# Optimization experiments

Hardware: AMD Instinct MI355X
Metric: run time of the kernel (lower is better)

Reference implementation:

```python
import jax, jax.numpy as jnp
from jax import lax
import numpy as np

EPS_BN = 1e-5


def _bn(x, g, b, axis):
    # eval-mode BatchNorm with running_mean=0, running_var=1
    shape = [1] * x.ndim
    shape[axis] = -1
    scale = (g / jnp.sqrt(1.0 + EPS_BN)).reshape(shape)
    return x * scale + b.reshape(shape)


def farthest_point_sample(xyz, npoint):
    B, N, _ = xyz.shape
    bidx = jnp.arange(B)

    def body(carry, _):
        dist, far = carry                      # [B,N], [B]
        centroid = xyz[bidx, far]              # [B,3]
        d = jnp.sum((xyz - centroid[:, None, :]) ** 2, axis=-1)
        dist = jnp.minimum(dist, d)
        return (dist, jnp.argmax(dist, axis=-1)), far

    init = (jnp.full((B, N), 1e10, xyz.dtype), jnp.zeros((B,), jnp.int32))
    _, idxs = lax.scan(body, init, None, length=npoint)
    return idxs.T                              # [B,npoint]


def square_distance(src, dst):
    # [B,S,3] x [B,N,3] -> [B,S,N]
    d = -2.0 * jnp.einsum('bsc,bnc->bsn', src, dst)
    d = d + jnp.sum(src ** 2, -1)[:, :, None] + jnp.sum(dst ** 2, -1)[:, None, :]
    return d


def sample_and_group(npoint, nsample, xyz, points):
    B = xyz.shape[0]
    bidx = jnp.arange(B)
    fps_idx = farthest_point_sample(xyz, npoint)          # [B,S]
    new_xyz = xyz[bidx[:, None], fps_idx]                 # [B,S,3]
    new_points = points[bidx[:, None], fps_idx]           # [B,S,C]
    dists = square_distance(new_xyz, xyz)                 # [B,S,N]
    _, idx = lax.top_k(-dists, nsample)                   # nearest nsample
    grouped = points[bidx[:, None, None], idx]            # [B,S,K,C]
    grouped_norm = grouped - new_points[:, :, None, :]
    rep = jnp.broadcast_to(new_points[:, :, None, :], grouped.shape)
    return new_xyz, jnp.concatenate([grouped_norm, rep], axis=-1)  # [B,S,K,2C]


def local_op(x, w, g, b):
    # x [B,S,K,D]; conv1d k=1 over channels D, BN, ReLU, max over K -> [B,out,S]
    y = jnp.einsum('bskd,od->bsko', x, w)
    y = jax.nn.relu(_bn(y, g, b, axis=3))
    y = jnp.max(y, axis=2)                                # [B,S,out]
    return jnp.transpose(y, (0, 2, 1))                    # [B,out,S]


def sa_layer(x, qk_w, v_w, v_b, t_w, t_b, g, b):
    # x [B,C,N]; q and k share weights (offset attention)
    xq = jnp.einsum('bcn,oc->bno', x, qk_w)               # [B,N,C/4]
    xk = jnp.einsum('bcn,oc->bon', x, qk_w)               # [B,C/4,N]
    xv = jnp.einsum('bcn,oc->bon', x, v_w) + v_b[:, None]
    energy = jnp.einsum('bnd,bdm->bnm', xq, xk)           # [B,N,N]
    attn = jax.nn.softmax(energy, axis=-1)
    attn = attn / (1e-9 + attn.sum(axis=1, keepdims=True))
    x_r = jnp.einsum('bcn,bnm->bcm', xv, attn)
    x_r = jnp.einsum('bcn,oc->bon', x - x_r, t_w) + t_b[:, None]
    x_r = jax.nn.relu(_bn(x_r, g, b, axis=1))
    return x + x_r


def setup_inputs() -> dict:
    key = jax.random.key(0)
    ks = iter(jax.random.split(key, 48))
    rn = lambda shape, s=0.05: jax.random.normal(next(ks), shape, jnp.float32) * s
    inp = {
        'xyz': jax.random.normal(next(ks), (32, 16384, 3), jnp.float32),
        'f': jax.random.normal(next(ks), (32, 16384, 3), jnp.float32),
        'conv1_w': rn((64, 6)), 'bn1_g': jnp.ones(64), 'bn1_b': jnp.zeros(64),
        'l0_w': rn((64, 128)), 'l0_g': jnp.ones(64), 'l0_b': jnp.zeros(64),
        'l1_w': rn((64, 128)), 'l1_g': jnp.ones(64), 'l1_b': jnp.zeros(64),
        'st_c1_w': rn((64, 64)), 'st_bn1_g': jnp.ones(64), 'st_bn1_b': jnp.zeros(64),
        'st_c2_w': rn((64, 64)), 'st_bn2_g': jnp.ones(64), 'st_bn2_b': jnp.zeros(64),
        'sa1_qk_w': rn((16, 64)), 'sa1_v_w': rn((64, 64)), 'sa1_v_b': jnp.zeros(64),
        'sa1_t_w': rn((64, 64)), 'sa1_t_b': jnp.zeros(64), 'sa1_g': jnp.ones(64), 'sa1_b': jnp.zeros(64),
        'sa2_qk_w': rn((16, 64)), 'sa2_v_w': rn((64, 64)), 'sa2_v_b': jnp.zeros(64),
        'sa2_t_w': rn((64, 64)), 'sa2_t_b': jnp.zeros(64), 'sa2_g': jnp.ones(64), 'sa2_b': jnp.zeros(64),
        'fuse_w': rn((256, 192)), 'fuse_g': jnp.ones(256), 'fuse_b': jnp.zeros(256),
        'lin1_w': rn((256, 256)), 'bn6_g': jnp.ones(256), 'bn6_b': jnp.zeros(256),
        'lin2_w': rn((256, 256)), 'lin2_b': jnp.zeros(256),
    }
    return inp


def _forward(xyz, f, conv1_w, bn1_g, bn1_b, l0_w, l0_g, l0_b, l1_w, l1_g, l1_b,
             st_c1_w, st_bn1_g, st_bn1_b, st_c2_w, st_bn2_g, st_bn2_b,
             sa1_qk_w, sa1_v_w, sa1_v_b, sa1_t_w, sa1_t_b, sa1_g, sa1_b,
             sa2_qk_w, sa2_v_w, sa2_v_b, sa2_t_w, sa2_t_b, sa2_g, sa2_b,
             fuse_w, fuse_g, fuse_b, lin1_w, bn6_g, bn6_b, lin2_w, lin2_b):
    center = jnp.mean(xyz, axis=1)                        # [B,3]
    xyz_c = xyz - center[:, None, :]
    pts = jnp.concatenate([xyz_c, f], axis=2)             # [B,N,6]
    geo = pts[..., :3]
    xin = jnp.transpose(pts, (0, 2, 1))                   # [B,6,N]
    x = jax.nn.relu(_bn(jnp.einsum('bcn,oc->bon', xin, conv1_w), bn1_g, bn1_b, 1))
    x = jnp.transpose(x, (0, 2, 1))                       # [B,N,64]
    new_xyz, nf = sample_and_group(128, 32, geo, x)
    feature_0 = local_op(nf, l0_w, l0_g, l0_b)            # [B,64,128]
    feature = jnp.transpose(feature_0, (0, 2, 1))
    _, nf2 = sample_and_group(32, 16, new_xyz, feature)
    feature_1 = local_op(nf2, l1_w, l1_g, l1_b)           # [B,64,32]
    # StackedAttention
    x = jax.nn.relu(_bn(jnp.einsum('bcn,oc->bon', feature_1, st_c1_w), st_bn1_g, st_bn1_b, 1))
    x = jax.nn.relu(_bn(jnp.einsum('bcn,oc->bon', x, st_c2_w), st_bn2_g, st_bn2_b, 1))
    x1 = sa_layer(x, sa1_qk_w, sa1_v_w, sa1_v_b, sa1_t_w, sa1_t_b, sa1_g, sa1_b)
    x2 = sa_layer(x1, sa2_qk_w, sa2_v_w, sa2_v_b, sa2_t_w, sa2_t_b, sa2_g, sa2_b)
    x = jnp.concatenate([x1, x2], axis=1)                 # [B,128,32]
    x = jnp.concatenate([x, feature_1], axis=1)           # [B,192,32]
    x = jax.nn.leaky_relu(_bn(jnp.einsum('bcn,oc->bon', x, fuse_w), fuse_g, fuse_b, 1), 0.2)
    x = jnp.max(x, axis=2)                                # [B,256]
    x = jax.nn.relu(_bn(x @ lin1_w.T, bn6_g, bn6_b, 1))   # dropout = identity (eval)
    x = x @ lin2_w.T + lin2_b
    return center, x


def reference(xyz, f, conv1_w, bn1_g, bn1_b, l0_w, l0_g, l0_b, l1_w, l1_g, l1_b,
              st_c1_w, st_bn1_g, st_bn1_b, st_c2_w, st_bn2_g, st_bn2_b,
              sa1_qk_w, sa1_v_w, sa1_v_b, sa1_t_w, sa1_t_b, sa1_g, sa1_b,
              sa2_qk_w, sa2_v_w, sa2_v_b, sa2_t_w, sa2_t_b, sa2_g, sa2_b,
              fuse_w, fuse_g, fuse_b, lin1_w, bn6_g, bn6_b, lin2_w, lin2_b):
    return _forward(xyz, f, conv1_w, bn1_g, bn1_b, l0_w, l0_g, l0_b, l1_w, l1_g, l1_b,
                    st_c1_w, st_bn1_g, st_bn1_b, st_c2_w, st_bn2_g, st_bn2_b,
                    sa1_qk_w, sa1_v_w, sa1_v_b, sa1_t_w, sa1_t_b, sa1_g, sa1_b,
                    sa2_qk_w, sa2_v_w, sa2_v_b, sa2_t_w, sa2_t_b, sa2_g, sa2_b,
                    fuse_w, fuse_g, fuse_b, lin1_w, bn6_g, bn6_b, lin2_w, lin2_b)
```

## Files before the change

kernel.cpp:

```cpp
#include <hip/hip_runtime.h>


__device__ __forceinline__ float bnscale(float g){ return g / sqrtf(1.0f + 1e-5f); }

__device__ __forceinline__ float conv_feat6(float p0,float p1,float p2,float p3,float p4,float p5,
                                            float w0,float w1,float w2,float w3,float w4,float w5,
                                            float sc,float bs){
    float y = p0*w0;
    y = fmaf(p1,w1,y); y = fmaf(p2,w2,y); y = fmaf(p3,w3,y);
    y = fmaf(p4,w4,y); y = fmaf(p5,w5,y);
    return fmaxf(fmaf(y,sc,bs), 0.0f);
}

__device__ __forceinline__ float fpsdist(float dx,float dy,float dz){
    #pragma clang fp contract(off)
    return (dx*dx + dy*dy) + dz*dz;
}

__device__ __forceinline__ float sumsq3(float x,float y,float z){
    #pragma clang fp contract(off)
    return (x*x + y*y) + z*z;
}
__device__ __forceinline__ float sqdist3(float qx,float qy,float qz,float qs,
                                         float px,float py,float pz){
    #pragma clang fp contract(off)
    {
        float dot = (qx*px + qy*py) + qz*pz;
        float pn  = (px*px + py*py) + pz*pz;
        return (-2.0f*dot + qs) + pn;
    }
}

__device__ __forceinline__ unsigned long long packdi(float d, unsigned int idx){
    unsigned int u = __float_as_uint(d);
    unsigned int msk = (unsigned int)((int)u >> 31);
    u ^= (msk | 0x80000000u);
    return ((unsigned long long)u << 32) | (unsigned long long)idx;
}

__device__ __forceinline__ unsigned long long u64min(unsigned long long a, unsigned long long b){
    return a < b ? a : b;
}

__device__ __forceinline__ unsigned long long u64_shfl_down(unsigned long long v, int off){
    unsigned int lo = (unsigned int)v, hi = (unsigned int)(v >> 32);
    lo = __shfl_down(lo, off, 64);
    hi = __shfl_down(hi, off, 64);
    return ((unsigned long long)hi << 32) | (unsigned long long)lo;
}

__device__ __forceinline__ unsigned long long u64_bcast0(unsigned long long v){
    unsigned int lo = (unsigned int)v, hi = (unsigned int)(v >> 32);
    lo = __shfl(lo, 0, 64);
    hi = __shfl(hi, 0, 64);
    return ((unsigned long long)hi << 32) | (unsigned long long)lo;
}

__global__ __launch_bounds__(512, 1) void k_fps1(const float* __restrict__ xyz,
                                                 float* __restrict__ center,
                                                 float* __restrict__ out,
                                                 int* __restrict__ idx_out){
    constexpr int NTH = 512, PPT = 32, N = 16384, NPOINT = 128, NW = 8;
    int b = blockIdx.x, t = threadIdx.x;
    int wid = t>>6, lane = t&63;

    __shared__ float s_red[NW][3];
    __shared__ unsigned int s_khi[2][NW], s_klo[2][NW];

    const float* xb = xyz + (size_t)b*N*3;
    float px[PPT], py[PPT], pz[PPT], dist[PPT];
    #pragma unroll
    for (int i=0;i<PPT;i++){
        const float* sp = xb + (size_t)(t + i*NTH)*3;
        px[i]=sp[0]; py[i]=sp[1]; pz[i]=sp[2];
        dist[i]=1e10f;
    }
    float sx=0.f, sy=0.f, sz=0.f;
    #pragma unroll
    for (int i=0;i<PPT;i++){ sx+=px[i]; sy+=py[i]; sz+=pz[i]; }
    #pragma unroll
    for (int off=32; off>=1; off>>=1){
        sx += __shfl_down(sx, off, 64);
        sy += __shfl_down(sy, off, 64);
        sz += __shfl_down(sz, off, 64);
    }
    if (lane==0){ s_red[wid][0]=sx; s_red[wid][1]=sy; s_red[wid][2]=sz; }
    __syncthreads();
    float cx0=0.f, cy0=0.f, cz0=0.f;
    #pragma unroll
    for (int w2=0; w2<NW; ++w2){ cx0+=s_red[w2][0]; cy0+=s_red[w2][1]; cz0+=s_red[w2][2]; }
    cx0 *= (1.0f/16384.0f); cy0 *= (1.0f/16384.0f); cz0 *= (1.0f/16384.0f);
    if (t < 3){
        float c = (t==0)?cx0:((t==1)?cy0:cz0);
        center[b*3+t] = c;
        out[b*3+t] = c;
    }
    #pragma unroll
    for (int i=0;i<PPT;i++){ px[i]-=cx0; py[i]-=cy0; pz[i]-=cz0; }
    if (t==0) idx_out[b*NPOINT] = 0;

    float cx = xb[0]-cx0, cy = xb[1]-cy0, cz = xb[2]-cz0;

    for (int it=1; it<NPOINT; ++it){
        int par = it & 1;
        float bv = -1.0f; int bis = 0;
        #pragma unroll
        for (int i=0;i<PPT;i++){
            float d = fpsdist(px[i]-cx, py[i]-cy, pz[i]-cz);
            float nd = fminf(dist[i], d);
            dist[i] = nd;
            bool better = nd > bv;
            bv  = better ? nd : bv;
            bis = better ? i  : bis;
        }
        int bi = t + (bis<<9);
        unsigned long long key = ((unsigned long long)__float_as_uint(bv) << 32)
                               | (unsigned long long)(unsigned)(~(unsigned)bi);
        #pragma unroll
        for (int off=32; off>=1; off>>=1){
            unsigned long long ok = u64_shfl_down(key, off);
            key = ok > key ? ok : key;
        }
        if (lane==0){ s_khi[par][wid]=(unsigned)(key>>32); s_klo[par][wid]=(unsigned)key; }
        __syncthreads();
        unsigned long long gk = ((unsigned long long)s_khi[par][0] << 32) | s_klo[par][0];
        #pragma unroll
        for (int w2=1; w2<NW; ++w2){
            unsigned long long k2 = ((unsigned long long)s_khi[par][w2] << 32) | s_klo[par][w2];
            if (k2 > gk) gk = k2;
        }
        int gi = (int)(~(unsigned)(gk & 0xFFFFFFFFull));
        gi = __builtin_amdgcn_readfirstlane(gi);
        if (t==0) idx_out[b*NPOINT + it] = gi;
        const float* wp = xb + (size_t)gi*3;
        cx = wp[0]-cx0; cy = wp[1]-cy0; cz = wp[2]-cz0;
    }
}

__global__ __launch_bounds__(256) void k_knn1(const float* __restrict__ xyz,
                                              const float* __restrict__ f,
                                              const float* __restrict__ center,
                                              const float* __restrict__ conv1_w,
                                              const float* __restrict__ bn1_g,
                                              const float* __restrict__ bn1_b,
                                              const int* __restrict__ fps_idx,
                                              float* __restrict__ new_xyz,
                                              float* __restrict__ np_feat,
                                              int* __restrict__ knn_idx){
    int t = threadIdx.x, wid = t>>6, lane = t&63;
    int q = blockIdx.x*4 + wid;
    int b = q>>7, s = q&127;

    float cx = center[b*3+0], cy = center[b*3+1], cz = center[b*3+2];
    int idx = fps_idx[b*128+s];
    const float* xp = xyz + ((size_t)b*16384 + idx)*3;
    const float* fp = f   + ((size_t)b*16384 + idx)*3;
    float p0 = xp[0]-cx, p1 = xp[1]-cy, p2 = xp[2]-cz;
    float p3 = fp[0], p4 = fp[1], p5 = fp[2];

    {
        const float* w6 = conv1_w + lane*6;
        float v = conv_feat6(p0,p1,p2,p3,p4,p5, w6[0],w6[1],w6[2],w6[3],w6[4],w6[5],
                             bnscale(bn1_g[lane]), bn1_b[lane]);
        np_feat[(size_t)q*64 + lane] = v;
        if (lane < 3){
            float pc = (lane==0)?p0:((lane==1)?p1:p2);
            new_xyz[(size_t)q*3 + lane] = pc;
        }
    }

    float qx = p0, qy = p1, qz = p2;
    float qs = sumsq3(qx,qy,qz);
    const float* xb = xyz + (size_t)b*16384*3;

    unsigned long long m0=~0ull, m1=~0ull, m2=~0ull, m3=~0ull;
    for (int i=0; i<256; i+=4){
        #pragma unroll
        for (int j=0;j<4;j++){
            int n = lane + ((i+j)<<6);
            const float* p = xb + (size_t)n*3;
            float dx = p[0]-cx, dy = p[1]-cy, dz = p[2]-cz;
            float d = sqdist3(qx,qy,qz,qs,dx,dy,dz);
            unsigned long long pk = packdi(d,(unsigned)n);
            if (j==0) m0 = u64min(m0,pk);
            else if (j==1) m1 = u64min(m1,pk);
            else if (j==2) m2 = u64min(m2,pk);
            else m3 = u64min(m3,pk);
        }
    }

    size_t kbase = (size_t)q*32;
    for (int r=0; r<32; ++r){
        unsigned long long mm = u64min(u64min(m0,m1), u64min(m2,m3));
        #pragma unroll
        for (int off=32; off>=1; off>>=1) mm = u64min(mm, u64_shfl_down(mm, off));
        unsigned long long win = u64_bcast0(mm);
        unsigned int widx = (unsigned int)(win & 0xFFFFFFFFull);
        if (lane==0) knn_idx[kbase + r] = (int)widx;
        int c = (int)(widx & 255u);
        int n2 = c + (lane<<8);
        const float* p = xb + (size_t)n2*3;
        float dx = p[0]-cx, dy = p[1]-cy, dz = p[2]-cz;
        float d = sqdist3(qx,qy,qz,qs,dx,dy,dz);
        unsigned long long pk = packdi(d,(unsigned)n2);
        if (pk <= win) pk = ~0ull;
        #pragma unroll
        for (int off=32; off>=1; off>>=1) pk = u64min(pk, u64_shfl_down(pk, off));
        unsigned long long nm = u64_bcast0(pk);
        int owner = c & 63, slot = c >> 6;
        if (lane == owner){
            if (slot==0) m0 = nm;
            else if (slot==1) m1 = nm;
            else if (slot==2) m2 = nm;
            else m3 = nm;
        }
    }
}

template<int K, int NQ, int NSRC, bool RECOMP>
__global__ __launch_bounds__(256, 2) void k_group_local(
    const float* __restrict__ xyz, const float* __restrict__ f, const float* __restrict__ center,
    const float* __restrict__ conv1_w, const float* __restrict__ bn1_g, const float* __restrict__ bn1_b,
    const float* __restrict__ src_feat,
    const int* __restrict__ knn_idx, const float* __restrict__ np_feat,
    const float* __restrict__ w, const float* __restrict__ g, const float* __restrict__ bb,
    float* __restrict__ out)
{
    __shared__ float wt[128*65];
    __shared__ float s_sc[64], s_bs[64];
    __shared__ float cwT[6*64];
    __shared__ float s_csc[64], s_cbs[64];
    __shared__ float np_l[4][64];
    __shared__ float gda[4][K][64];
    __shared__ float s_pts[4][K][6];

    int t = threadIdx.x;
    for (int e=t; e<8192; e+=256){ int o = e>>7, d = e&127; wt[d*65 + o] = w[e]; }
    if (t < 64){ s_sc[t] = bnscale(g[t]); s_bs[t] = bb[t]; }
    if constexpr (RECOMP){
        for (int e=t; e<384; e+=256){ int o = e/6, j = e%6; cwT[j*64 + o] = conv1_w[e]; }
        if (t < 64){ s_csc[t] = bnscale(bn1_g[t]); s_cbs[t] = bn1_b[t]; }
    }
    __syncthreads();

    int wid = t>>6, lane = t&63;
    int q = blockIdx.x*4 + wid;
    int b = q / NQ, s = q % NQ;

    float np_o = np_feat[((size_t)b*NQ + s)*64 + lane];
    np_l[wid][lane] = np_o;

    const int* kix = knn_idx + ((size_t)b*NQ + s)*K;

    if constexpr (RECOMP){
        float cx = center[b*3+0], cy = center[b*3+1], cz = center[b*3+2];
        if (lane < K){
            int myi = kix[lane];
            const float* xp = xyz + ((size_t)b*16384 + myi)*3;
            s_pts[wid][lane][0] = xp[0]-cx;
            s_pts[wid][lane][1] = xp[1]-cy;
            s_pts[wid][lane][2] = xp[2]-cz;
            const float* fp = f + ((size_t)b*16384 + myi)*3;
            s_pts[wid][lane][3] = fp[0];
            s_pts[wid][lane][4] = fp[1];
            s_pts[wid][lane][5] = fp[2];
        }
        #pragma unroll
        for (int k=0; k<K; ++k){
            float gv = conv_feat6(s_pts[wid][k][0], s_pts[wid][k][1], s_pts[wid][k][2],
                                  s_pts[wid][k][3], s_pts[wid][k][4], s_pts[wid][k][5],
                                  cwT[0*64+lane], cwT[1*64+lane], cwT[2*64+lane],
                                  cwT[3*64+lane], cwT[4*64+lane], cwT[5*64+lane],
                                  s_csc[lane], s_cbs[lane]);
            gda[wid][k][lane] = gv - np_o;
        }
    } else {
        int myi = kix[lane < K ? lane : 0];
        #pragma unroll
        for (int k=0; k<K; ++k){
            int ik = __shfl(myi, k, 64);
            gda[wid][k][lane] = src_feat[((size_t)b*NSRC + ik)*64 + lane] - np_o;
        }
    }

    float C = 0.f;
    #pragma unroll
    for (int d=0; d<64; d++) C = fmaf(np_l[wid][d], wt[(64+d)*65 + lane], C);

    float acc_y[K];
    #pragma unroll
    for (int k=0;k<K;k++) acc_y[k] = C;

    #pragma unroll
    for (int c=0; c<2; ++c){
        float wr[32];
        #pragma unroll
        for (int j=0;j<32;j++) wr[j] = wt[(c*32+j)*65 + lane];
        #pragma unroll
        for (int k=0;k<K;k++){
            const float4* g4 = (const float4*)&gda[wid][k][c*32];
            float yk = 0.f;
            #pragma unroll
            for (int j4=0;j4<8;j4++){
                float4 gg = g4[j4];
                yk = fmaf(gg.x, wr[j4*4+0], yk);
                yk = fmaf(gg.y, wr[j4*4+1], yk);
                yk = fmaf(gg.z, wr[j4*4+2], yk);
                yk = fmaf(gg.w, wr[j4*4+3], yk);
            }
            acc_y[k] = acc_y[k] + yk;
        }
    }

    float acc = -1e30f;
    #pragma unroll
    for (int k=0;k<K;k++){
        float v = fmaxf(fmaf(acc_y[k], s_sc[lane], s_bs[lane]), 0.0f);
        acc = fmaxf(acc, v);
    }
    out[((size_t)b*NQ + s)*64 + lane] = acc;
}

__device__ void sa_block(const float* X, float* Xout,
                         float* Q, float* E, float* XV, float* XR, float* CS,
                         const float* qk_w, const float* v_w, const float* v_b,
                         const float* t_w, const float* t_b,
                         const float* g, const float* bb, int t)
{
    for (int e=t; e<512; e+=256){
        int n = e>>4, o = e&15;
        float y = 0.f;
        for (int c=0;c<64;c++) y = fmaf(qk_w[o*64+c], X[c*32+n], y);
        Q[n*16+o] = y;
    }
    for (int e=t; e<2048; e+=256){
        int o = e>>5, n = e&31;
        float y = v_b[o];
        for (int c=0;c<64;c++) y = fmaf(v_w[o*64+c], X[c*32+n], y);
        XV[o*32+n] = y;
    }
    __syncthreads();
    for (int e=t; e<1024; e+=256){
        int n = e>>5, m = e&31;
        float y = 0.f;
        for (int d=0;d<16;d++) y = fmaf(Q[n*16+d], Q[m*16+d], y);
        E[e] = y;
    }
    __syncthreads();
    if (t < 32){
        float mx = -1e30f;
        for (int m=0;m<32;m++) mx = fmaxf(mx, E[t*32+m]);
        float sum = 0.f;
        for (int m=0;m<32;m++){ float v = expf(E[t*32+m]-mx); E[t*32+m]=v; sum += v; }
        for (int m=0;m<32;m++) E[t*32+m] = E[t*32+m] / sum;
    }
    __syncthreads();
    if (t < 32){
        float cs = 0.f;
        for (int n=0;n<32;n++) cs += E[n*32+t];
        CS[t] = 1e-9f + cs;
    }
    __syncthreads();
    for (int e=t; e<1024; e+=256) E[e] = E[e] / CS[e&31];
    __syncthreads();
    for (int e=t; e<2048; e+=256){
        int c = e>>5, m = e&31;
        float y = 0.f;
        for (int n=0;n<32;n++) y = fmaf(XV[c*32+n], E[n*32+m], y);
        XR[c*32+m] = y;
    }
    __syncthreads();
    for (int e=t; e<2048; e+=256){
        int o = e>>5, n = e&31;
        float y = 0.f;
        for (int c=0;c<64;c++) y = fmaf(t_w[o*64+c], X[c*32+n]-XR[c*32+n], y);
        y += t_b[o];
        y = fmaxf(fmaf(y, bnscale(g[o]), bb[o]), 0.0f);
        Xout[e] = X[e] + y;
    }
    __syncthreads();
}

__global__ __launch_bounds__(256) void k_mega(
    const float* __restrict__ new_xyz1,
    const float* __restrict__ feat,
    const float* __restrict__ l1_w, const float* __restrict__ l1_g, const float* __restrict__ l1_b,
    const float* st_c1_w, const float* st_bn1_g, const float* st_bn1_b,
    const float* st_c2_w, const float* st_bn2_g, const float* st_bn2_b,
    const float* sa1_qk, const float* sa1_v, const float* sa1_vb,
    const float* sa1_t, const float* sa1_tb, const float* sa1_g, const float* sa1_b,
    const float* sa2_qk, const float* sa2_v, const float* sa2_vb,
    const float* sa2_t, const float* sa2_tb, const float* sa2_g, const float* sa2_b,
    const float* fuse_w, const float* fuse_g, const float* fuse_b,
    const float* lin1_w, const float* bn6_g, const float* bn6_b,
    const float* lin2_w, const float* lin2_b,
    float* __restrict__ out)
{
    __shared__ float nx1[384];
    __shared__ int   s_i2[32];
    __shared__ float np2L[2048];
    __shared__ float nx2[96];
    __shared__ int   s_k2[512];
    __shared__ float wt[8320];
    __shared__ float s_sc[64], s_bs[64];
    __shared__ float gdaL[4][16][64];
    __shared__ float smt[14848];

    int b = blockIdx.x, t = threadIdx.x, wid = t>>6, lane = t&63;

    for (int e=t; e<384; e+=256) nx1[e] = new_xyz1[(size_t)b*384 + e];
    for (int e=t; e<8192; e+=256){ int o = e>>7, d = e&127; wt[d*65 + o] = l1_w[e]; }
    if (t < 64){ s_sc[t] = bnscale(l1_g[t]); s_bs[t] = l1_b[t]; }
    __syncthreads();

    if (wid == 0){
        float px[2],py[2],pz[2],dist[2];
        #pragma unroll
        for (int i=0;i<2;i++){
            int n = lane + i*64;
            px[i]=nx1[n*3+0]; py[i]=nx1[n*3+1]; pz[i]=nx1[n*3+2];
            dist[i]=1e10f;
        }
        if (lane==0) s_i2[0] = 0;
        float cx=nx1[0], cy=nx1[1], cz=nx1[2];
        for (int it=1; it<32; ++it){
            float bv=-1.0f; int bi=0;
            float bx=0.f, by=0.f, bz=0.f;
            #pragma unroll
            for (int i=0;i<2;i++){
                float d = fpsdist(px[i]-cx, py[i]-cy, pz[i]-cz);
                float nd = fminf(dist[i], d);
                dist[i]=nd;
                bool better = nd > bv;
                bv = better ? nd : bv;
                bi = better ? (lane + i*64) : bi;
                bx = better ? px[i] : bx;
                by = better ? py[i] : by;
                bz = better ? pz[i] : bz;
            }
            unsigned long long key = ((unsigned long long)__float_as_uint(bv) << 32)
                                   | (unsigned long long)(unsigned)(~(unsigned)bi);
            #pragma unroll
            for (int off=32; off>=1; off>>=1){
                unsigned long long ok = u64_shfl_down(key, off);
                float ox = __shfl_down(bx, off, 64);
                float oy = __shfl_down(by, off, 64);
                float oz = __shfl_down(bz, off, 64);
                bool better = ok > key;
                key = better ? ok : key;
                bx = better ? ox : bx;
                by = better ? oy : by;
                bz = better ? oz : bz;
            }
            key = u64_bcast0(key);
            cx = __shfl(bx, 0, 64); cy = __shfl(by, 0, 64); cz = __shfl(bz, 0, 64);
            if (lane==0) s_i2[it] = (int)(~(unsigned)(key & 0xFFFFFFFFull));
        }
    }
    __syncthreads();

    for (int e=t; e<2048; e+=256){
        int s = e>>6, o = e&63;
        np2L[s*64 + o] = feat[((size_t)b*128 + s_i2[s])*64 + o];
    }
    if (t < 32){
        int idx = s_i2[t];
        nx2[t*3+0] = nx1[idx*3+0];
        nx2[t*3+1] = nx1[idx*3+1];
        nx2[t*3+2] = nx1[idx*3+2];
    }
    __syncthreads();

    for (int j=0;j<8;j++){
        int s = wid + 4*j;
        float qx = nx2[s*3+0], qy = nx2[s*3+1], qz = nx2[s*3+2];
        float qs = sumsq3(qx,qy,qz);
        unsigned long long pp0, pp1;
        {
            float ax=nx1[lane*3+0], ay=nx1[lane*3+1], az=nx1[lane*3+2];
            pp0 = packdi(sqdist3(qx,qy,qz,qs,ax,ay,az), (unsigned)lane);
            ax=nx1[(lane+64)*3+0]; ay=nx1[(lane+64)*3+1]; az=nx1[(lane+64)*3+2];
            pp1 = packdi(sqdist3(qx,qy,qz,qs,ax,ay,az), (unsigned)(lane+64));
        }
        for (int r=0; r<16; ++r){
            unsigned long long mm = u64min(pp0, pp1);
            #pragma unroll
            for (int off=32; off>=1; off>>=1) mm = u64min(mm, u64_shfl_down(mm, off));
            unsigned long long win = u64_bcast0(mm);
            if (lane==0) s_k2[s*16 + r] = (int)(win & 0xFFFFFFFFull);
            if (pp0 == win) pp0 = ~0ull;
            if (pp1 == win) pp1 = ~0ull;
        }
    }
    __syncthreads();

    for (int j=0;j<8;j++){
        int s = wid + 4*j;
        float np_o = np2L[s*64 + lane];
        #pragma unroll
        for (int k=0;k<16;k++){
            int ik = s_k2[s*16 + k];
            gdaL[wid][k][lane] = feat[((size_t)b*128 + ik)*64 + lane] - np_o;
        }
        float C0 = 0.f;
        #pragma unroll
        for (int d=0; d<64; d++) C0 = fmaf(np2L[s*64 + d], wt[(64+d)*65 + lane], C0);
        float acc_y[16];
        #pragma unroll
        for (int k=0;k<16;k++) acc_y[k] = C0;
        #pragma unroll
        for (int c=0; c<2; ++c){
            float wr[32];
            #pragma unroll
            for (int jj=0;jj<32;jj++) wr[jj] = wt[(c*32+jj)*65 + lane];
            #pragma unroll
            for (int k=0;k<16;k++){
                const float4* g4 = (const float4*)&gdaL[wid][k][c*32];
                float yk = 0.f;
                #pragma unroll
                for (int j4=0;j4<8;j4++){
                    float4 gg = g4[j4];
                    yk = fmaf(gg.x, wr[j4*4+0], yk);
                    yk = fmaf(gg.y, wr[j4*4+1], yk);
                    yk = fmaf(gg.z, wr[j4*4+2], yk);
                    yk = fmaf(gg.w, wr[j4*4+3], yk);
                }
                acc_y[k] = acc_y[k] + yk;
            }
        }
        float acc = -1e30f;
        #pragma unroll
        for (int k=0;k<16;k++){
            float v = fmaxf(fmaf(acc_y[k], s_sc[lane], s_bs[lane]), 0.0f);
            acc = fmaxf(acc, v);
        }
        smt[lane*32 + s] = acc;
    }
    __syncthreads();

    float* F1 = smt;
    float* XA = smt + 2048;
    float* XB = smt + 4096;
    float* Q  = smt + 6144;
    float* E  = smt + 6656;
    float* XV = smt + 7680;
    float* XR = smt + 9728;
    float* CS = smt + 11776;
    float* FO = smt + 6144;
    float* PO = smt + 14336;
    float* P2 = smt + 14592;

    for (int e=t; e<2048; e+=256){
        int o = e>>5, n = e&31;
        float y = 0.f;
        for (int c=0;c<64;c++) y = fmaf(st_c1_w[o*64+c], F1[c*32+n], y);
        XA[e] = fmaxf(fmaf(y, bnscale(st_bn1_g[o]), st_bn1_b[o]), 0.0f);
    }
    __syncthreads();
    for (int e=t; e<2048; e+=256){
        int o = e>>5, n = e&31;
        float y = 0.f;
        for (int c=0;c<64;c++) y = fmaf(st_c2_w[o*64+c], XA[c*32+n], y);
        XB[e] = fmaxf(fmaf(y, bnscale(st_bn2_g[o]), st_bn2_b[o]), 0.0f);
    }
    __syncthreads();
    sa_block(XB, XA, Q,E,XV,XR,CS, sa1_qk, sa1_v, sa1_vb, sa1_t, sa1_tb, sa1_g, sa1_b, t);
    sa_block(XA, XB, Q,E,XV,XR,CS, sa2_qk, sa2_v, sa2_vb, sa2_t, sa2_tb, sa2_g, sa2_b, t);
    for (int e=t; e<8192; e+=256){
        int o = e>>5, n = e&31;
        const float* wr = fuse_w + o*192;
        float y = 0.f;
        for (int c=0;c<64;c++) y = fmaf(wr[c],      XA[c*32+n], y);
        for (int c=0;c<64;c++) y = fmaf(wr[64+c],   XB[c*32+n], y);
        for (int c=0;c<64;c++) y = fmaf(wr[128+c],  F1[c*32+n], y);
        float v = fmaf(y, bnscale(fuse_g[o]), fuse_b[o]);
        FO[e] = (v > 0.0f) ? v : 0.2f*v;
    }
    __syncthreads();
    {
        float mx = -1e30f;
        for (int n=0;n<32;n++) mx = fmaxf(mx, FO[t*32+n]);
        PO[t] = mx;
    }
    __syncthreads();
    {
        const float* wr = lin1_w + t*256;
        float y = 0.f;
        for (int c=0;c<256;c++) y = fmaf(wr[c], PO[c], y);
        P2[t] = fmaxf(fmaf(y, bnscale(bn6_g[t]), bn6_b[t]), 0.0f);
    }
    __syncthreads();
    {
        const float* wr = lin2_w + t*256;
        float y = 0.f;
        for (int c=0;c<256;c++) y = fmaf(wr[c], P2[c], y);
        out[96 + b*256 + t] = y + lin2_b[t];
    }
}

extern "C" void kernel_launch(void* const* d_in, const int* in_sizes, int n_in,
                              void* d_out, int out_size, void* d_ws, size_t ws_size,
                              hipStream_t stream)
{
    const float* xyz      = (const float*)d_in[0];
    const float* f        = (const float*)d_in[1];
    const float* conv1_w  = (const float*)d_in[2];
    const float* bn1_g    = (const float*)d_in[3];
    const float* bn1_b    = (const float*)d_in[4];
    const float* l0_w     = (const float*)d_in[5];
    const float* l0_g     = (const float*)d_in[6];
    const float* l0_b     = (const float*)d_in[7];
    const float* l1_w     = (const float*)d_in[8];
    const float* l1_g     = (const float*)d_in[9];
    const float* l1_b     = (const float*)d_in[10];
    const float* st_c1_w  = (const float*)d_in[11];
    const float* st_bn1_g = (const float*)d_in[12];
    const float* st_bn1_b = (const float*)d_in[13];
    const float* st_c2_w  = (const float*)d_in[14];
    const float* st_bn2_g = (const float*)d_in[15];
    const float* st_bn2_b = (const float*)d_in[16];
    const float* sa1_qk   = (const float*)d_in[17];
    const float* sa1_v    = (const float*)d_in[18];
    const float* sa1_vb   = (const float*)d_in[19];
    const float* sa1_t    = (const float*)d_in[20];
    const float* sa1_tb   = (const float*)d_in[21];
    const float* sa1_g    = (const float*)d_in[22];
    const float* sa1_b    = (const float*)d_in[23];
    const float* sa2_qk   = (const float*)d_in[24];
    const float* sa2_v    = (const float*)d_in[25];
    const float* sa2_vb   = (const float*)d_in[26];
    const float* sa2_t    = (const float*)d_in[27];
    const float* sa2_tb   = (const float*)d_in[28];
    const float* sa2_g    = (const float*)d_in[29];
    const float* sa2_b    = (const float*)d_in[30];
    const float* fuse_w   = (const float*)d_in[31];
    const float* fuse_g   = (const float*)d_in[32];
    const float* fuse_b   = (const float*)d_in[33];
    const float* lin1_w   = (const float*)d_in[34];
    const float* bn6_g    = (const float*)d_in[35];
    const float* bn6_b    = (const float*)d_in[36];
    const float* lin2_w   = (const float*)d_in[37];
    const float* lin2_b   = (const float*)d_in[38];
    float* out = (float*)d_out;

    float* ws = (float*)d_ws;
    float* center   = ws + 0;
    float* new_xyz1 = ws + 96;
    float* np1      = ws + 12384;
    float* feat     = ws + 274528;
    int*   fps1     = (int*)(ws + 536672);
    int*   knn1     = (int*)(ws + 540768);

    k_fps1<<<32, 512, 0, stream>>>(xyz, center, out, fps1);
    k_knn1<<<1024, 256, 0, stream>>>(xyz, f, center, conv1_w, bn1_g, bn1_b,
                                     fps1, new_xyz1, np1, knn1);
    k_group_local<32,128,1,true><<<1024, 256, 0, stream>>>(
        xyz, f, center, conv1_w, bn1_g, bn1_b, nullptr, knn1, np1, l0_w, l0_g, l0_b, feat);
    k_mega<<<32, 256, 0, stream>>>(new_xyz1, feat,
        l1_w, l1_g, l1_b,
        st_c1_w, st_bn1_g, st_bn1_b, st_c2_w, st_bn2_g, st_bn2_b,
        sa1_qk, sa1_v, sa1_vb, sa1_t, sa1_tb, sa1_g, sa1_b,
        sa2_qk, sa2_v, sa2_vb, sa2_t, sa2_tb, sa2_g, sa2_b,
        fuse_w, fuse_g, fuse_b, lin1_w, bn6_g, bn6_b, lin2_w, lin2_b, out);
}
```

Measured before the change: 729.5 us.

## Widen FPS and mega kernels to 1024 threads with shuffle-based softmax

Doubles the FPS block to 1024 threads with 16 points per thread, and quadruples the mega kernel block to 1024 threads. The grid has only 32 blocks, so the aim is more parallelism per block to cut the latency of the serial FPS loop and the tail network. The attention softmax now uses wave shuffles instead of a 32-thread serial loop. Shared buffers are re-laid out with padded strides (33) to avoid bank conflicts, and the gathered-feature buffer is reused in halves. Risks are more waves taking part in each block-wide barrier and higher register pressure under the 1024-thread launch bounds.

```diff
diff --git a/kernel.cpp b/kernel.cpp
--- a/kernel.cpp
+++ b/kernel.cpp
@@ -56,11 +56,11 @@
     return ((unsigned long long)hi << 32) | (unsigned long long)lo;
 }
 
-__global__ __launch_bounds__(512, 1) void k_fps1(const float* __restrict__ xyz,
-                                                 float* __restrict__ center,
-                                                 float* __restrict__ out,
-                                                 int* __restrict__ idx_out){
-    constexpr int NTH = 512, PPT = 32, N = 16384, NPOINT = 128, NW = 8;
+__global__ __launch_bounds__(1024, 1) void k_fps1(const float* __restrict__ xyz,
+                                                  float* __restrict__ center,
+                                                  float* __restrict__ out,
+                                                  int* __restrict__ idx_out){
+    constexpr int NTH = 1024, PPT = 16, N = 16384, NPOINT = 128, NW = 16;
     int b = blockIdx.x, t = threadIdx.x;
     int wid = t>>6, lane = t&63;
 
@@ -113,7 +113,7 @@
             bv  = better ? nd : bv;
             bis = better ? i  : bis;
         }
-        int bi = t + (bis<<9);
+        int bi = t + (bis<<10);
         unsigned long long key = ((unsigned long long)__float_as_uint(bv) << 32)
                                | (unsigned long long)(unsigned)(~(unsigned)bi);
         #pragma unroll
@@ -327,32 +327,37 @@
                          const float* t_w, const float* t_b,
                          const float* g, const float* bb, int t)
 {
-    for (int e=t; e<512; e+=256){
+    constexpr int NT = 1024;
+    for (int e=t; e<512; e+=NT){
         int n = e>>4, o = e&15;
         float y = 0.f;
         for (int c=0;c<64;c++) y = fmaf(qk_w[o*64+c], X[c*32+n], y);
         Q[n*16+o] = y;
     }
-    for (int e=t; e<2048; e+=256){
+    for (int e=t; e<2048; e+=NT){
         int o = e>>5, n = e&31;
         float y = v_b[o];
         for (int c=0;c<64;c++) y = fmaf(v_w[o*64+c], X[c*32+n], y);
         XV[o*32+n] = y;
     }
     __syncthreads();
-    for (int e=t; e<1024; e+=256){
-        int n = e>>5, m = e&31;
+    {
+        int n = t>>5, m = t&31;
         float y = 0.f;
         for (int d=0;d<16;d++) y = fmaf(Q[n*16+d], Q[m*16+d], y);
-        E[e] = y;
-    }
-    __syncthreads();
-    if (t < 32){
-        float mx = -1e30f;
-        for (int m=0;m<32;m++) mx = fmaxf(mx, E[t*32+m]);
-        float sum = 0.f;
-        for (int m=0;m<32;m++){ float v = expf(E[t*32+m]-mx); E[t*32+m]=v; sum += v; }
-        for (int m=0;m<32;m++) E[t*32+m] = E[t*32+m] / sum;
+        E[t] = y;
+    }
+    __syncthreads();
+    {
+        float v = E[t];
+        float mx = v;
+        #pragma unroll
+        for (int mk=16; mk>=1; mk>>=1) mx = fmaxf(mx, __shfl_xor(mx, mk, 64));
+        float p = expf(v - mx);
+        float sum = p;
+        #pragma unroll
+        for (int mk=16; mk>=1; mk>>=1) sum += __shfl_xor(sum, mk, 64);
+        E[t] = p / sum;
     }
     __syncthreads();
     if (t < 32){
@@ -361,16 +366,16 @@
         CS[t] = 1e-9f + cs;
     }
     __syncthreads();
-    for (int e=t; e<1024; e+=256) E[e] = E[e] / CS[e&31];
-    __syncthreads();
-    for (int e=t; e<2048; e+=256){
+    E[t] = E[t] / CS[t&31];
+    __syncthreads();
+    for (int e=t; e<2048; e+=NT){
         int c = e>>5, m = e&31;
         float y = 0.f;
         for (int n=0;n<32;n++) y = fmaf(XV[c*32+n], E[n*32+m], y);
         XR[c*32+m] = y;
     }
     __syncthreads();
-    for (int e=t; e<2048; e+=256){
+    for (int e=t; e<2048; e+=NT){
         int o = e>>5, n = e&31;
         float y = 0.f;
         for (int c=0;c<64;c++) y = fmaf(t_w[o*64+c], X[c*32+n]-XR[c*32+n], y);
@@ -381,7 +386,7 @@
     __syncthreads();
 }
 
-__global__ __launch_bounds__(256) void k_mega(
+__global__ __launch_bounds__(1024) void k_mega(
     const float* __restrict__ new_xyz1,
     const float* __restrict__ feat,
     const float* __restrict__ l1_w, const float* __restrict__ l1_g, const float* __restrict__ l1_b,
@@ -396,6 +401,7 @@
     const float* lin2_w, const float* lin2_b,
     float* __restrict__ out)
 {
+    constexpr int NT = 1024;
     __shared__ float nx1[384];
     __shared__ int   s_i2[32];
     __shared__ float np2L[2048];
@@ -403,13 +409,12 @@
     __shared__ int   s_k2[512];
     __shared__ float wt[8320];
     __shared__ float s_sc[64], s_bs[64];
-    __shared__ float gdaL[4][16][64];
-    __shared__ float smt[14848];
+    __shared__ float smt[15168];
 
     int b = blockIdx.x, t = threadIdx.x, wid = t>>6, lane = t&63;
 
-    for (int e=t; e<384; e+=256) nx1[e] = new_xyz1[(size_t)b*384 + e];
-    for (int e=t; e<8192; e+=256){ int o = e>>7, d = e&127; wt[d*65 + o] = l1_w[e]; }
+    for (int e=t; e<384; e+=NT) nx1[e] = new_xyz1[(size_t)b*384 + e];
+    for (int e=t; e<8192; e+=NT){ int o = e>>7, d = e&127; wt[d*65 + o] = l1_w[e]; }
     if (t < 64){ s_sc[t] = bnscale(l1_g[t]); s_bs[t] = l1_b[t]; }
     __syncthreads();
 
@@ -459,7 +464,7 @@
     }
     __syncthreads();
 
-    for (int e=t; e<2048; e+=256){
+    for (int e=t; e<2048; e+=NT){
         int s = e>>6, o = e&63;
         np2L[s*64 + o] = feat[((size_t)b*128 + s_i2[s])*64 + o];
     }
@@ -471,8 +476,8 @@
     }
     __syncthreads();
 
-    for (int j=0;j<8;j++){
-        int s = wid + 4*j;
+    for (int j=0;j<2;j++){
+        int s = wid + 16*j;
         float qx = nx2[s*3+0], qy = nx2[s*3+1], qz = nx2[s*3+2];
         float qs = sumsq3(qx,qy,qz);
         unsigned long long pp0, pp1;
@@ -494,14 +499,10 @@
     }
     __syncthreads();
 
-    for (int j=0;j<8;j++){
-        int s = wid + 4*j;
+    float* gda = smt + 2112;
+    for (int j=0;j<2;j++){
+        int s = wid + 16*j;
         float np_o = np2L[s*64 + lane];
-        #pragma unroll
-        for (int k=0;k<16;k++){
-            int ik = s_k2[s*16 + k];
-            gdaL[wid][k][lane] = feat[((size_t)b*128 + ik)*64 + lane] - np_o;
-        }
         float C0 = 0.f;
         #pragma unroll
         for (int d=0; d<64; d++) C0 = fmaf(np2L[s*64 + d], wt[(64+d)*65 + lane], C0);
@@ -509,23 +510,31 @@
         #pragma unroll
         for (int k=0;k<16;k++) acc_y[k] = C0;
         #pragma unroll
-        for (int c=0; c<2; ++c){
-            float wr[32];
+        for (int half=0; half<2; ++half){
             #pragma unroll
-            for (int jj=0;jj<32;jj++) wr[jj] = wt[(c*32+jj)*65 + lane];
+            for (int kk=0;kk<8;++kk){
+                int ik = s_k2[s*16 + half*8 + kk];
+                gda[(wid*8+kk)*64 + lane] = feat[((size_t)b*128 + ik)*64 + lane] - np_o;
+            }
             #pragma unroll
-            for (int k=0;k<16;k++){
-                const float4* g4 = (const float4*)&gdaL[wid][k][c*32];
-                float yk = 0.f;
+            for (int c=0; c<2; ++c){
+                float wr[32];
                 #pragma unroll
-                for (int j4=0;j4<8;j4++){
-                    float4 gg = g4[j4];
-                    yk = fmaf(gg.x, wr[j4*4+0], yk);
-                    yk = fmaf(gg.y, wr[j4*4+1], yk);
-                    yk = fmaf(gg.z, wr[j4*4+2], yk);
-                    yk = fmaf(gg.w, wr[j4*4+3], yk);
+                for (int jj=0;jj<32;jj++) wr[jj] = wt[(c*32+jj)*65 + lane];
+                #pragma unroll
+                for (int kk=0;kk<8;++kk){
+                    const float4* g4 = (const float4*)&gda[(wid*8+kk)*64 + c*32];
+                    float yk = 0.f;
+                    #pragma unroll
+                    for (int j4=0;j4<8;j4++){
+                        float4 gg = g4[j4];
+                        yk = fmaf(gg.x, wr[j4*4+0], yk);
+                        yk = fmaf(gg.y, wr[j4*4+1], yk);
+                        yk = fmaf(gg.z, wr[j4*4+2], yk);
+                        yk = fmaf(gg.w, wr[j4*4+3], yk);
+                    }
+                    acc_y[half*8+kk] = acc_y[half*8+kk] + yk;
                 }
-                acc_y[k] = acc_y[k] + yk;
             }
         }
         float acc = -1e30f;
@@ -534,30 +543,30 @@
             float v = fmaxf(fmaf(acc_y[k], s_sc[lane], s_bs[lane]), 0.0f);
             acc = fmaxf(acc, v);
         }
-        smt[lane*32 + s] = acc;
+        smt[lane*33 + s] = acc;
     }
     __syncthreads();
 
     float* F1 = smt;
-    float* XA = smt + 2048;
-    float* XB = smt + 4096;
-    float* Q  = smt + 6144;
-    float* E  = smt + 6656;
-    float* XV = smt + 7680;
-    float* XR = smt + 9728;
-    float* CS = smt + 11776;
-    float* FO = smt + 6144;
-    float* PO = smt + 14336;
-    float* P2 = smt + 14592;
-
-    for (int e=t; e<2048; e+=256){
+    float* XA = smt + 2112;
+    float* XB = smt + 4160;
+    float* Q  = smt + 6208;
+    float* E  = smt + 6720;
+    float* XV = smt + 7744;
+    float* XR = smt + 9792;
+    float* CS = smt + 11840;
+    float* FO = smt + 6208;
+    float* PO = smt + 14656;
+    float* P2 = smt + 14912;
+
+    for (int e=t; e<2048; e+=NT){
         int o = e>>5, n = e&31;
         float y = 0.f;
-        for (int c=0;c<64;c++) y = fmaf(st_c1_w[o*64+c], F1[c*32+n], y);
+        for (int c=0;c<64;c++) y = fmaf(st_c1_w[o*64+c], F1[c*33+n], y);
         XA[e] = fmaxf(fmaf(y, bnscale(st_bn1_g[o]), st_bn1_b[o]), 0.0f);
     }
     __syncthreads();
-    for (int e=t; e<2048; e+=256){
+    for (int e=t; e<2048; e+=NT){
         int o = e>>5, n = e&31;
         float y = 0.f;
         for (int c=0;c<64;c++) y = fmaf(st_c2_w[o*64+c], XA[c*32+n], y);
@@ -566,31 +575,31 @@
     __syncthreads();
     sa_block(XB, XA, Q,E,XV,XR,CS, sa1_qk, sa1_v, sa1_vb, sa1_t, sa1_tb, sa1_g, sa1_b, t);
     sa_block(XA, XB, Q,E,XV,XR,CS, sa2_qk, sa2_v, sa2_vb, sa2_t, sa2_tb, sa2_g, sa2_b, t);
-    for (int e=t; e<8192; e+=256){
+    for (int e=t; e<8192; e+=NT){
         int o = e>>5, n = e&31;
         const float* wr = fuse_w + o*192;
         float y = 0.f;
         for (int c=0;c<64;c++) y = fmaf(wr[c],      XA[c*32+n], y);
         for (int c=0;c<64;c++) y = fmaf(wr[64+c],   XB[c*32+n], y);
-        for (int c=0;c<64;c++) y = fmaf(wr[128+c],  F1[c*32+n], y);
+        for (int c=0;c<64;c++) y = fmaf(wr[128+c],  F1[c*33+n], y);
         float v = fmaf(y, bnscale(fuse_g[o]), fuse_b[o]);
-        FO[e] = (v > 0.0f) ? v : 0.2f*v;
-    }
-    __syncthreads();
-    {
+        FO[o*33+n] = (v > 0.0f) ? v : 0.2f*v;
+    }
+    __syncthreads();
+    if (t < 256){
         float mx = -1e30f;
-        for (int n=0;n<32;n++) mx = fmaxf(mx, FO[t*32+n]);
+        for (int n=0;n<32;n++) mx = fmaxf(mx, FO[t*33+n]);
         PO[t] = mx;
     }
     __syncthreads();
-    {
+    if (t < 256){
         const float* wr = lin1_w + t*256;
         float y = 0.f;
         for (int c=0;c<256;c++) y = fmaf(wr[c], PO[c], y);
         P2[t] = fmaxf(fmaf(y, bnscale(bn6_g[t]), bn6_b[t]), 0.0f);
     }
     __syncthreads();
-    {
+    if (t < 256){
         const float* wr = lin2_w + t*256;
         float y = 0.f;
         for (int c=0;c<256;c++) y = fmaf(wr[c], P2[c], y);
@@ -651,12 +660,12 @@
     int*   fps1     = (int*)(ws + 536672);
     int*   knn1     = (int*)(ws + 540768);
 
-    k_fps1<<<32, 512, 0, stream>>>(xyz, center, out, fps1);
+    k_fps1<<<32, 1024, 0, stream>>>(xyz, center, out, fps1);
     k_knn1<<<1024, 256, 0, stream>>>(xyz, f, center, conv1_w, bn1_g, bn1_b,
                                      fps1, new_xyz1, np1, knn1);
     k_group_local<32,128,1,true><<<1024, 256, 0, stream>>>(
         xyz, f, center, conv1_w, bn1_g, bn1_b, nullptr, knn1, np1, l0_w, l0_g, l0_b, feat);
-    k_mega<<<32, 256, 0, stream>>>(new_xyz1, feat,
+    k_mega<<<32, 1024, 0, stream>>>(new_xyz1, feat,
         l1_w, l1_g, l1_b,
         st_c1_w, st_bn1_g, st_bn1_b, st_c2_w, st_bn2_g, st_bn2_b,
         sa1_qk, sa1_v, sa1_vb, sa1_t, sa1_tb, sa1_g, sa1_b,
```

Result: no change. 724.3 us (-0.7%).
